# Performance work log

Hardware: AMD Instinct MI355X
Metric: run time of the kernel (lower is better)

Reference implementation:

```python
import jax, jax.numpy as jnp
import numpy as np

N = 100000
E = 1600000
F = 64
THETA = (0.6, -0.4, 0.3, -0.2, 0.1)  # k = 5 polynomial coefficients


def setup_inputs() -> dict:
    key = jax.random.key(0)
    kx, ke = jax.random.split(key)
    x = jax.random.normal(kx, (N, F), dtype=jnp.float32)
    edge_index = jax.random.randint(ke, (2, E), 0, N, dtype=jnp.int64)
    return {"x": x, "edge_index": edge_index}


def _l_sym_mul(feat, src, dst, deg_inv_sqrt, n):
    # L_sym * feat = feat - D^{-1/2} A D^{-1/2} feat
    src_norm = feat[src] * deg_inv_sqrt[src]            # [E, F] gather + scale
    agg = jax.ops.segment_sum(src_norm, dst, num_segments=n)  # scatter-add to dst
    return feat - deg_inv_sqrt * agg


def reference(x, edge_index):
    src, dst = edge_index[0], edge_index[1]
    n = x.shape[0]
    # in-degree from dst, clamp to >= 1, D^{-1/2} as [N, 1]
    deg = jax.ops.segment_sum(jnp.ones((src.shape[0],), dtype=x.dtype), dst,
                              num_segments=n)
    deg = jnp.maximum(deg, 1.0)[:, None]
    deg_inv_sqrt = deg ** -0.5

    h_acc = THETA[0] * x
    feat = x
    for k in range(1, len(THETA)):
        feat = _l_sym_mul(feat, src, dst, deg_inv_sqrt, n)
        h_acc = h_acc + THETA[k] * feat
    return h_acc
```

## Files before the change

kernel.cpp:

```cpp
#include <hip/hip_runtime.h>
#include <hip/hip_fp16.h>


constexpr int kF = 64;
constexpr int BSHIFT = 8;
constexpr int NB = 1 << BSHIFT;
constexpr int TILEA = 8192;
constexpr int KMAX = 512;

typedef unsigned nv4u __attribute__((ext_vector_type(4)));
typedef float    nv4f __attribute__((ext_vector_type(4)));

static __device__ __forceinline__ float hlo(unsigned u) {
    return __half2float(__ushort_as_half((unsigned short)(u & 0xffffu)));
}
static __device__ __forceinline__ float hhi(unsigned u) {
    return __half2float(__ushort_as_half((unsigned short)(u >> 16)));
}
static __device__ __forceinline__ unsigned pack2h(float a, float b) {
    return (unsigned)__half_as_ushort(__float2half_rn(a)) |
           ((unsigned)__half_as_ushort(__float2half_rn(b)) << 16);
}
static __device__ __forceinline__ unsigned padd2(unsigned a, unsigned b) {
    __half2 ha = *reinterpret_cast<__half2*>(&a);
    __half2 hb = *reinterpret_cast<__half2*>(&b);
    __half2 hc = __hadd2(ha, hb);
    return *reinterpret_cast<unsigned*>(&hc);
}

__global__ void k_binA(const int* __restrict__ src, const int* __restrict__ dst,
                       unsigned* __restrict__ pairs, int* __restrict__ gcursor,
                       const float4* __restrict__ x4, uint4* __restrict__ xb4,
                       int n8, int E, int K, int cap) {
    __shared__ unsigned stage[TILEA];
    __shared__ unsigned short stageB[TILEA];
    __shared__ int hist[KMAX];
    __shared__ int lb[KMAX];
    __shared__ int gb[KMAX];
    const int tid = threadIdx.x;
    const long long tb = (long long)blockIdx.x * TILEA;
    const int tcount = (int)min((long long)TILEA, (long long)E - tb);

    {
        int per = (n8 + gridDim.x - 1) / (int)gridDim.x;
        int b0 = blockIdx.x * per;
        int b1 = min(b0 + per, n8);
        for (int i = b0 + tid; i < b1; i += 512) {
            float4 a = x4[2 * i];
            float4 b = x4[2 * i + 1];
            uint4 o;
            o.x = pack2h(a.x, a.y);
            o.y = pack2h(a.z, a.w);
            o.z = pack2h(b.x, b.y);
            o.w = pack2h(b.z, b.w);
            xb4[i] = o;
        }
    }

    hist[tid] = 0;
    __syncthreads();
    int dc[16], sc[16];
    #pragma unroll
    for (int k = 0; k < 16; ++k) {
        int i = tid + k * 512;
        if (i < tcount) {
            dc[k] = dst[tb + i];
            sc[k] = src[tb + i];
            atomicAdd(&hist[dc[k] >> BSHIFT], 1);
        } else {
            dc[k] = -1;
        }
    }
    __syncthreads();
    const int cnt = hist[tid];
    lb[tid] = cnt;
    __syncthreads();
    for (int o = 1; o < KMAX; o <<= 1) {
        int t = (tid >= o) ? lb[tid - o] : 0;
        __syncthreads();
        lb[tid] += t;
        __syncthreads();
    }
    const int excl = lb[tid] - cnt;
    __syncthreads();
    lb[tid] = excl;
    gb[tid] = (tid < K && cnt > 0) ? atomicAdd(&gcursor[tid], cnt) : 0;
    hist[tid] = excl;
    __syncthreads();
    #pragma unroll
    for (int k = 0; k < 16; ++k) {
        if (dc[k] >= 0) {
            int d = dc[k];
            int b = d >> BSHIFT;
            int pos = atomicAdd(&hist[b], 1);
            stage[pos]  = ((unsigned)(d & (NB - 1)) << 23) | (unsigned)sc[k];
            stageB[pos] = (unsigned short)b;
        }
    }
    __syncthreads();
    for (int j = tid; j < tcount; j += 512) {
        int b = stageB[j];
        pairs[(size_t)b * cap + gb[b] + (j - lb[b])] = stage[j];
    }
}

__global__ void k_binB(const unsigned* __restrict__ pairs, const int* __restrict__ gcursor,
                       int* __restrict__ rp, float* __restrict__ dinv2,
                       float* __restrict__ rdeg, int* __restrict__ csr,
                       int* __restrict__ csr0,
                       const uint4* __restrict__ xb, uint4* __restrict__ g0,
                       int N, int E, int K, int cap) {
    __shared__ int gsc[KMAX];
    __shared__ int cnt[NB];
    __shared__ int stmp[NB];
    __shared__ int cur[NB];
    __shared__ float sdinv[NB];
    const int b = blockIdx.x;
    const int tid = threadIdx.x;

    if (b == 0 && tid < 8)
        g0[((size_t)N << 3) + tid] = make_uint4(0, 0, 0, 0);

    int gv = (tid < K) ? gcursor[tid] : 0;
    gsc[tid] = gv;
    __syncthreads();
    for (int o = 1; o < KMAX; o <<= 1) {
        int t = (tid >= o) ? gsc[tid - o] : 0;
        __syncthreads();
        gsc[tid] += t;
        __syncthreads();
    }
    const int ecnt = gcursor[b];
    const int base = gsc[b] - ecnt;
    const unsigned* bp = pairs + (size_t)b * cap;

    if (tid < NB) cnt[tid] = 0;
    __syncthreads();
    for (int i = tid; i < ecnt; i += 512)
        atomicAdd(&cnt[bp[i] >> 23], 1);
    __syncthreads();
    int v = (tid < NB) ? cnt[tid] : 0;
    if (tid < NB) stmp[tid] = v;
    __syncthreads();
    for (int o = 1; o < NB; o <<= 1) {
        int t = (tid >= o && tid < NB) ? stmp[tid - o] : 0;
        __syncthreads();
        if (tid < NB) stmp[tid] += t;
        __syncthreads();
    }
    int node = (b << BSHIFT) + tid;
    if (tid < NB) {
        int abs0 = base + stmp[tid] - v;
        cur[tid] = abs0;
        float d = fmaxf((float)v, 1.0f);
        sdinv[tid] = rsqrtf(d);
        if (node < N) {
            rp[node] = abs0;
            dinv2[node] = 1.0f / d;
            rdeg[node]  = sqrtf(d);
        }
    }
    if (b == K - 1 && tid == 0) rp[N] = E;
    __syncthreads();
    for (int i = tid; i < ecnt; i += 512) {
        unsigned p = bp[i];
        int pos = atomicAdd(&cur[p >> 23], 1);
        csr[pos] = (int)(p & 0x7FFFFFu);
    }
    __syncthreads();
    if (tid < NB && node < N) {
        int abs0 = base + stmp[tid] - v;
        int4 q0, q1;
        q0.x = (0 < v) ? csr[abs0 + 0] : N;
        q0.y = (1 < v) ? csr[abs0 + 1] : N;
        q0.z = (2 < v) ? csr[abs0 + 2] : N;
        q0.w = (3 < v) ? csr[abs0 + 3] : N;
        q1.x = (4 < v) ? csr[abs0 + 4] : N;
        q1.y = (5 < v) ? csr[abs0 + 5] : N;
        q1.z = (6 < v) ? csr[abs0 + 6] : N;
        q1.w = (7 < v) ? csr[abs0 + 7] : N;
        *(int4*)(csr0 + ((size_t)node << 3))     = q0;
        *(int4*)(csr0 + ((size_t)node << 3) + 4) = q1;
    }
    const int nbase = b << BSHIFT;
    const int qmax = min(NB, N - nbase) << 3;
    const uint4* xbp = xb + ((size_t)nbase << 3);
    uint4* g0p = g0 + ((size_t)nbase << 3);
    for (int q = tid; q < qmax; q += 512) {
        float di = sdinv[q >> 3];
        uint4 xv = xbp[q];
        uint4 o;
        o.x = pack2h(di * hlo(xv.x), di * hhi(xv.x));
        o.y = pack2h(di * hlo(xv.y), di * hhi(xv.y));
        o.z = pack2h(di * hlo(xv.z), di * hhi(xv.z));
        o.w = pack2h(di * hlo(xv.w), di * hhi(xv.w));
        g0p[q] = o;
    }
}

template <bool LAST>
__global__ void k_gather(const int* __restrict__ rp, const int* __restrict__ csr,
                         const int* __restrict__ csr0,
                         const unsigned short* __restrict__ gin,
                         const float* __restrict__ dinv2,
                         unsigned short* __restrict__ gout,
                         const unsigned short* __restrict__ xb,
                         const unsigned short* __restrict__ g1t,
                         const unsigned short* __restrict__ g2t,
                         const float* __restrict__ rdeg,
                         float* __restrict__ h, int n,
                         float t0, float t1, float t2, float t3, float t4) {
    if (!LAST && blockIdx.x == 0 && threadIdx.x < 8)
        *(((uint4*)(gout + ((size_t)n << 6))) + threadIdx.x) = make_uint4(0, 0, 0, 0);

    int wid = (blockIdx.x * blockDim.x + threadIdx.x) >> 6;
    int lane = threadIdx.x & 63;
    int half = lane >> 5;
    int r = (lane >> 3) & 3;
    int c = lane & 7;
    int node = wid * 2 + half;
    if (wid * 2 >= n) return;
    bool valid = node < n;

    int s1 = n, s2 = n;
    if (valid) {
        s1 = csr0[((size_t)node << 3) + r];
        s2 = csr0[((size_t)node << 3) + r + 4];
    }
    int beg = valid ? rp[node] : 0;
    int end = valid ? rp[node + 1] : 0;

    const bool ep = (r == 0) && valid;
    size_t off = ((size_t)node << 6) + (c << 3);
    uint4 rr = make_uint4(0, 0, 0, 0);
    float d2 = 0.f, rd = 0.f;
    nv4u xv = {0u, 0u, 0u, 0u}, aa = {0u, 0u, 0u, 0u}, bb = {0u, 0u, 0u, 0u};
    if (ep) {
        rr = *(const uint4*)(gin + off);
        d2 = dinv2[node];
        if (LAST) {
            xv = __builtin_nontemporal_load((const nv4u*)(xb + off));
            aa = __builtin_nontemporal_load((const nv4u*)(g1t + off));
            bb = __builtin_nontemporal_load((const nv4u*)(g2t + off));
            rd = rdeg[node];
        }
    }

    int len = end - beg;
    int olen = __shfl_xor(len, 32, 64);
    int mlen = (len > olen) ? len : olen;

    unsigned acc[4] = {0u, 0u, 0u, 0u};

    uint4 rc1 = *(const uint4*)(gin + ((size_t)s1 << 6) + (c << 3));
    uint4 rc2 = *(const uint4*)(gin + ((size_t)s2 << 6) + (c << 3));
    int sn1 = n, sn2 = n;
    {
        int j1b = beg + 8 + r, j2b = j1b + 4;
        bool vb = 8 < mlen;
        bool b1 = vb && (j1b < end), b2 = vb && (j2b < end);
        sn1 = csr[b1 ? j1b : 0]; sn1 = b1 ? sn1 : n;
        sn2 = csr[b2 ? j2b : 0]; sn2 = b2 ? sn2 : n;
    }
    for (int i = 0; i < mlen; i += 8) {
        uint4 rn1 = *(const uint4*)(gin + ((size_t)sn1 << 6) + (c << 3));
        uint4 rn2 = *(const uint4*)(gin + ((size_t)sn2 << 6) + (c << 3));
        int j1n = beg + i + 16 + r, j2n = j1n + 4;
        bool vn = (i + 16) < mlen;
        bool t1c = vn && (j1n < end), t2c = vn && (j2n < end);
        int st1 = csr[t1c ? j1n : 0]; st1 = t1c ? st1 : n;
        int st2 = csr[t2c ? j2n : 0]; st2 = t2c ? st2 : n;
        acc[0] = padd2(acc[0], rc1.x); acc[1] = padd2(acc[1], rc1.y);
        acc[2] = padd2(acc[2], rc1.z); acc[3] = padd2(acc[3], rc1.w);
        acc[0] = padd2(acc[0], rc2.x); acc[1] = padd2(acc[1], rc2.y);
        acc[2] = padd2(acc[2], rc2.z); acc[3] = padd2(acc[3], rc2.w);
        rc1 = rn1; rc2 = rn2;
        sn1 = st1; sn2 = st2;
    }
    #pragma unroll
    for (int m = 8; m <= 16; m <<= 1) {
        #pragma unroll
        for (int i = 0; i < 4; ++i)
            acc[i] = padd2(acc[i], __shfl_xor(acc[i], m, 64));
    }

    if (ep) {
        float v[8];
        v[0] = hlo(rr.x) - d2 * hlo(acc[0]); v[1] = hhi(rr.x) - d2 * hhi(acc[0]);
        v[2] = hlo(rr.y) - d2 * hlo(acc[1]); v[3] = hhi(rr.y) - d2 * hhi(acc[1]);
        v[4] = hlo(rr.z) - d2 * hlo(acc[2]); v[5] = hhi(rr.z) - d2 * hhi(acc[2]);
        v[6] = hlo(rr.w) - d2 * hlo(acc[3]); v[7] = hhi(rr.w) - d2 * hhi(acc[3]);
        if (!LAST) {
            nv4u o;
            o.x = pack2h(v[0], v[1]);
            o.y = pack2h(v[2], v[3]);
            o.z = pack2h(v[4], v[5]);
            o.w = pack2h(v[6], v[7]);
            __builtin_nontemporal_store(o, (nv4u*)(gout + off));
        } else {
            float s1f = rd * t1, s2f = rd * t2, s3f = rd * t3, s4f = rd * t4;
            nv4f h0, h1;
            h0.x = t0 * hlo(xv.x) + s1f * hlo(aa.x) + s2f * hlo(bb.x) + s3f * hlo(rr.x) + s4f * v[0];
            h0.y = t0 * hhi(xv.x) + s1f * hhi(aa.x) + s2f * hhi(bb.x) + s3f * hhi(rr.x) + s4f * v[1];
            h0.z = t0 * hlo(xv.y) + s1f * hlo(aa.y) + s2f * hlo(bb.y) + s3f * hlo(rr.y) + s4f * v[2];
            h0.w = t0 * hhi(xv.y) + s1f * hhi(aa.y) + s2f * hhi(bb.y) + s3f * hhi(rr.y) + s4f * v[3];
            h1.x = t0 * hlo(xv.z) + s1f * hlo(aa.z) + s2f * hlo(bb.z) + s3f * hlo(rr.z) + s4f * v[4];
            h1.y = t0 * hhi(xv.z) + s1f * hhi(aa.z) + s2f * hhi(bb.z) + s3f * hhi(rr.z) + s4f * v[5];
            h1.z = t0 * hlo(xv.w) + s1f * hlo(aa.w) + s2f * hlo(bb.w) + s3f * hlo(rr.w) + s4f * v[6];
            h1.w = t0 * hhi(xv.w) + s1f * hhi(aa.w) + s2f * hhi(bb.w) + s3f * hhi(rr.w) + s4f * v[7];
            __builtin_nontemporal_store(h0, (nv4f*)(h + off));
            __builtin_nontemporal_store(h1, (nv4f*)(h + off + 4));
        }
    }
}

extern "C" void kernel_launch(void* const* d_in, const int* in_sizes, int n_in,
                              void* d_out, int out_size, void* d_ws, size_t ws_size,
                              hipStream_t stream) {
    const float* x  = (const float*)d_in[0];
    const int*   ei = (const int*)d_in[1];
    const int N = in_sizes[0] / kF;
    const int E = in_sizes[1] / 2;
    const int* src = ei;
    const int* dst = ei + E;
    float* h = (float*)d_out;

    const int K = (N + NB - 1) >> BSHIFT;
    const int cap = 2 * ((E + K - 1) / K);

    char* ws = (char*)d_ws;
    size_t off = 0;
    auto carve = [&](size_t bytes) {
        void* p = ws + off;
        off = (off + bytes + 511) & ~(size_t)511;
        return p;
    };
    size_t gbytes = (size_t)(N + 1) * kF * 2;
    int*            gcursor = (int*)carve((size_t)KMAX * 4);
    int*            rp      = (int*)carve((size_t)(N + 1) * 4);
    float*          dinv2   = (float*)carve((size_t)N * 4);
    float*          rdeg    = (float*)carve((size_t)N * 4);
    int*            csr     = (int*)carve((size_t)E * 4);
    int*            csr0    = (int*)carve((size_t)N * 8 * 4);
    unsigned short* xb      = (unsigned short*)carve((size_t)N * kF * 2);
    unsigned short* g0      = (unsigned short*)carve(gbytes);
    size_t pbytes = (size_t)K * cap * 4;
    unsigned short* g1      = (unsigned short*)carve(gbytes > pbytes ? gbytes : pbytes);
    unsigned short* g2      = (unsigned short*)carve(gbytes);
    unsigned short* g3      = (unsigned short*)carve(gbytes);
    unsigned*       pairs   = (unsigned*)g1;

    const float theta[5] = {0.6f, -0.4f, 0.3f, -0.2f, 0.1f};
    const int n8 = N * kF / 8;

    hipMemsetAsync(gcursor, 0, (size_t)KMAX * 4, stream);
    k_binA<<<(E + TILEA - 1) / TILEA, 512, 0, stream>>>(src, dst, pairs, gcursor,
                                                        (const float4*)x, (uint4*)xb,
                                                        n8, E, K, cap);
    k_binB<<<K, 512, 0, stream>>>(pairs, gcursor, rp, dinv2, rdeg, csr, csr0,
                                  (const uint4*)xb, (uint4*)g0, N, E, K, cap);

    const int nwaves = (N + 1) / 2;
    const int gblocks = (nwaves + 3) / 4;
    k_gather<false><<<gblocks, 256, 0, stream>>>(rp, csr, csr0, g0, dinv2, g1,
                                                 nullptr, nullptr, nullptr, nullptr,
                                                 nullptr, N, 0, 0, 0, 0, 0);
    k_gather<false><<<gblocks, 256, 0, stream>>>(rp, csr, csr0, g1, dinv2, g2,
                                                 nullptr, nullptr, nullptr, nullptr,
                                                 nullptr, N, 0, 0, 0, 0, 0);
    k_gather<false><<<gblocks, 256, 0, stream>>>(rp, csr, csr0, g2, dinv2, g3,
                                                 nullptr, nullptr, nullptr, nullptr,
                                                 nullptr, N, 0, 0, 0, 0, 0);
    k_gather<true><<<gblocks, 256, 0, stream>>>(rp, csr, csr0, g3, dinv2, nullptr,
                                                xb, g1, g2, rdeg, h, N,
                                                theta[0], theta[1], theta[2],
                                                theta[3], theta[4]);
}
```

Baseline: 237.7 us.

## Move x fp16 conversion into binB and halve binA tile size

The fp32-to-fp16 conversion of x moves from the edge-binning kernel into the per-bucket kernel. There it is fused with computing the degree-scaled g0, so x is read once in fp32 and the fp16 copy of xb is no longer re-read. The binning tile is halved to 4096 edges per block, which doubles the number of binA blocks to spread the load. The cost is more global atomics on the bucket cursors and smaller per-block runs when writing pairs.

New measurement: 235.9 us (median of 2 runs). Within noise of the previous version (-0.8%).

```diff
diff --git a/kernel.cpp b/kernel.cpp
--- a/kernel.cpp
+++ b/kernel.cpp
@@ -5,7 +5,7 @@
 constexpr int kF = 64;
 constexpr int BSHIFT = 8;
 constexpr int NB = 1 << BSHIFT;
-constexpr int TILEA = 8192;
+constexpr int TILEA = 4096;
 constexpr int KMAX = 512;
 
 typedef unsigned nv4u __attribute__((ext_vector_type(4)));
@@ -30,8 +30,7 @@
 
 __global__ void k_binA(const int* __restrict__ src, const int* __restrict__ dst,
                        unsigned* __restrict__ pairs, int* __restrict__ gcursor,
-                       const float4* __restrict__ x4, uint4* __restrict__ xb4,
-                       int n8, int E, int K, int cap) {
+                       int E, int K, int cap) {
     __shared__ unsigned stage[TILEA];
     __shared__ unsigned short stageB[TILEA];
     __shared__ int hist[KMAX];
@@ -41,27 +40,11 @@
     const long long tb = (long long)blockIdx.x * TILEA;
     const int tcount = (int)min((long long)TILEA, (long long)E - tb);
 
-    {
-        int per = (n8 + gridDim.x - 1) / (int)gridDim.x;
-        int b0 = blockIdx.x * per;
-        int b1 = min(b0 + per, n8);
-        for (int i = b0 + tid; i < b1; i += 512) {
-            float4 a = x4[2 * i];
-            float4 b = x4[2 * i + 1];
-            uint4 o;
-            o.x = pack2h(a.x, a.y);
-            o.y = pack2h(a.z, a.w);
-            o.z = pack2h(b.x, b.y);
-            o.w = pack2h(b.z, b.w);
-            xb4[i] = o;
-        }
-    }
-
     hist[tid] = 0;
     __syncthreads();
-    int dc[16], sc[16];
+    int dc[8], sc[8];
     #pragma unroll
-    for (int k = 0; k < 16; ++k) {
+    for (int k = 0; k < 8; ++k) {
         int i = tid + k * 512;
         if (i < tcount) {
             dc[k] = dst[tb + i];
@@ -88,7 +71,7 @@
     hist[tid] = excl;
     __syncthreads();
     #pragma unroll
-    for (int k = 0; k < 16; ++k) {
+    for (int k = 0; k < 8; ++k) {
         if (dc[k] >= 0) {
             int d = dc[k];
             int b = d >> BSHIFT;
@@ -108,7 +91,8 @@
                        int* __restrict__ rp, float* __restrict__ dinv2,
                        float* __restrict__ rdeg, int* __restrict__ csr,
                        int* __restrict__ csr0,
-                       const uint4* __restrict__ xb, uint4* __restrict__ g0,
+                       const float4* __restrict__ x4,
+                       uint4* __restrict__ xb4, uint4* __restrict__ g0,
                        int N, int E, int K, int cap) {
     __shared__ int gsc[KMAX];
     __shared__ int cnt[NB];
@@ -184,17 +168,24 @@
     }
     const int nbase = b << BSHIFT;
     const int qmax = min(NB, N - nbase) << 3;
-    const uint4* xbp = xb + ((size_t)nbase << 3);
     uint4* g0p = g0 + ((size_t)nbase << 3);
     for (int q = tid; q < qmax; q += 512) {
+        int gq = ((nbase + (q >> 3)) << 3) + (q & 7);
+        float4 a = x4[2 * gq];
+        float4 bb = x4[2 * gq + 1];
+        uint4 xo;
+        xo.x = pack2h(a.x, a.y);
+        xo.y = pack2h(a.z, a.w);
+        xo.z = pack2h(bb.x, bb.y);
+        xo.w = pack2h(bb.z, bb.w);
+        xb4[gq] = xo;
         float di = sdinv[q >> 3];
-        uint4 xv = xbp[q];
-        uint4 o;
-        o.x = pack2h(di * hlo(xv.x), di * hhi(xv.x));
-        o.y = pack2h(di * hlo(xv.y), di * hhi(xv.y));
-        o.z = pack2h(di * hlo(xv.z), di * hhi(xv.z));
-        o.w = pack2h(di * hlo(xv.w), di * hhi(xv.w));
-        g0p[q] = o;
+        uint4 go;
+        go.x = pack2h(di * a.x, di * a.y);
+        go.y = pack2h(di * a.z, di * a.w);
+        go.z = pack2h(di * bb.x, di * bb.y);
+        go.w = pack2h(di * bb.z, di * bb.w);
+        g0p[q] = go;
     }
 }
 
@@ -351,14 +342,13 @@
     unsigned*       pairs   = (unsigned*)g1;
 
     const float theta[5] = {0.6f, -0.4f, 0.3f, -0.2f, 0.1f};
-    const int n8 = N * kF / 8;
 
     hipMemsetAsync(gcursor, 0, (size_t)KMAX * 4, stream);
     k_binA<<<(E + TILEA - 1) / TILEA, 512, 0, stream>>>(src, dst, pairs, gcursor,
-                                                        (const float4*)x, (uint4*)xb,
-                                                        n8, E, K, cap);
+                                                        E, K, cap);
     k_binB<<<K, 512, 0, stream>>>(pairs, gcursor, rp, dinv2, rdeg, csr, csr0,
-                                  (const uint4*)xb, (uint4*)g0, N, E, K, cap);
+                                  (const float4*)x, (uint4*)xb, (uint4*)g0,
+                                  N, E, K, cap);
 
     const int nwaves = (N + 1) / 2;
     const int gblocks = (nwaves + 3) / 4;
```
